# Optimization experiments

Hardware: AMD Instinct MI355X
Metric: run time of the kernel (lower is better)

The kernel has to match this reference:

```python
import jax, jax.numpy as jnp
import numpy as np
import math

B, T, D, H, L = 8, 1024, 128, 8, 2
DH = D // H            # head dim = 16
F = 2 * D              # ffn hidden = 256 (FFN_EXPANSION=2)
SCALE = math.sqrt(DH)  # sqrt of Q last dim per head


def layernorm(x, g, b):
    m = jnp.mean(x, axis=-1, keepdims=True)
    v = jnp.var(x, axis=-1, keepdims=True)
    return (x - m) * jax.lax.rsqrt(v + 1e-5) * g + b


def setup_inputs() -> dict:
    key = jax.random.key(0)
    ks = jax.random.split(key, 16)
    s = 1.0 / math.sqrt(D)
    r = lambda i, shp: jax.random.normal(ks[i], shp, dtype=jnp.float32) * s
    return {
        "x": jax.random.normal(ks[0], (B, T, D), dtype=jnp.float32),
        "y": jax.random.normal(ks[1], (B, T, D), dtype=jnp.float32),
        # shared qkv projections (no bias), per layer
        "Wq": r(2, (L, D, D)), "Wk": r(3, (L, D, D)), "Wv": r(4, (L, D, D)),
        "Wox": r(5, (L, D, D)), "box": jnp.zeros((L, D), jnp.float32),
        "Woy": r(6, (L, D, D)), "boy": jnp.zeros((L, D), jnp.float32),
        "ln1x_g": jnp.ones((L, D), jnp.float32), "ln1x_b": jnp.zeros((L, D), jnp.float32),
        "ln1y_g": jnp.ones((L, D), jnp.float32), "ln1y_b": jnp.zeros((L, D), jnp.float32),
        "ln2x_g": jnp.ones((L, D), jnp.float32), "ln2x_b": jnp.zeros((L, D), jnp.float32),
        "ln2y_g": jnp.ones((L, D), jnp.float32), "ln2y_b": jnp.zeros((L, D), jnp.float32),
        "fx_w1": r(7, (L, D, F)), "fx_b1": jnp.zeros((L, F), jnp.float32),
        "fx_w2": r(8, (L, F, D)), "fx_b2": jnp.zeros((L, D), jnp.float32),
        "fy_w1": r(9, (L, D, F)), "fy_b1": jnp.zeros((L, F), jnp.float32),
        "fy_w2": r(10, (L, F, D)), "fy_b2": jnp.zeros((L, D), jnp.float32),
    }


def _heads(t):
    # (B,T,D) -> (B,T,H,DH)
    return t.reshape(B, T, H, DH)


def _block(x, y, Wq, Wk, Wv, Wox, box, Woy, boy,
           ln1x_g, ln1x_b, ln1y_g, ln1y_b, ln2x_g, ln2x_b, ln2y_g, ln2y_b,
           fx_w1, fx_b1, fx_w2, fx_b2, fy_w1, fy_b1, fy_w2, fy_b2):
    xn = layernorm(x, ln1x_g, ln1x_b)
    yn = layernorm(y, ln1y_g, ln1y_b)
    # x-branch: Q from y, K/V from x ; y-branch: Q from x, K/V from y
    qx = _heads(yn @ Wq); kx = _heads(xn @ Wk); vx = _heads(xn @ Wv)
    qy = _heads(xn @ Wq); ky = _heads(yn @ Wk); vy = _heads(yn @ Wv)
    ax = jnp.einsum('bthd,bshd->bhts', qx, kx)  # (B,H,T,T)
    ay = jnp.einsum('bthd,bshd->bhts', qy, ky)
    # cat over heads + reshape(B,2,H,T,T) + mean(dim=1) == per-head average
    w = jax.nn.softmax((ax + ay) * (0.5 / SCALE), axis=-1)
    o1 = jnp.einsum('bhts,bshd->bthd', w, vx).reshape(B, T, D) @ Wox + box
    o2 = jnp.einsum('bhts,bshd->bthd', w, vy).reshape(B, T, D) @ Woy + boy
    x = x + o1
    y = y + o2
    xn2 = layernorm(x, ln2x_g, ln2x_b)
    yn2 = layernorm(y, ln2y_g, ln2y_b)
    x = x + jax.nn.gelu(xn2 @ fx_w1 + fx_b1, approximate=False) @ fx_w2 + fx_b2
    y = y + jax.nn.gelu(yn2 @ fy_w1 + fy_b1, approximate=False) @ fy_w2 + fy_b2
    return x, y


def reference(x, y, Wq, Wk, Wv, Wox, box, Woy, boy,
              ln1x_g, ln1x_b, ln1y_g, ln1y_b, ln2x_g, ln2x_b, ln2y_g, ln2y_b,
              fx_w1, fx_b1, fx_w2, fx_b2, fy_w1, fy_b1, fy_w2, fy_b2):
    for i in range(L):
        x, y = _block(x, y, Wq[i], Wk[i], Wv[i], Wox[i], box[i], Woy[i], boy[i],
                      ln1x_g[i], ln1x_b[i], ln1y_g[i], ln1y_b[i],
                      ln2x_g[i], ln2x_b[i], ln2y_g[i], ln2y_b[i],
                      fx_w1[i], fx_b1[i], fx_w2[i], fx_b2[i],
                      fy_w1[i], fy_b1[i], fy_w2[i], fy_b2[i])
    return (x, y)
```

## Files before the change

kernel.cpp:

```cpp
#include <hip/hip_runtime.h>
#include <cstddef>

#define BB   8
#define TT   1024
#define DDIM 128
#define HH   8
#define DHH  16
#define FF   256
#define BT   (BB * TT)

typedef unsigned short u16;
typedef __attribute__((ext_vector_type(8))) short short8;
typedef __attribute__((ext_vector_type(4))) float f32x4;

__device__ __forceinline__ u16 bf(float x) {
  unsigned u = __builtin_bit_cast(unsigned, x);
  u += 0x7fffu + ((u >> 16) & 1u);
  return (u16)(u >> 16);
}
__device__ __forceinline__ u16 bft(float x) {
  return (u16)(__builtin_bit_cast(unsigned, x) >> 16);
}
__device__ __forceinline__ float gelu_f(float x) {
  const float t = x * (0.79788456f + 0.03567740814f * x * x);
  return x / (1.0f + __expf(-2.0f * t));
}

struct PrepP { const float* W; u16* Wt; int K; int N; };
struct PrepArgs { PrepP p[18]; };

__global__ __launch_bounds__(256) void prep_k(PrepArgs a) {
  const PrepP pp = a.p[blockIdx.z];
  const int n0 = blockIdx.x * 64, k0 = blockIdx.y * 64;
  if (n0 >= pp.N || k0 >= pp.K) return;
  __shared__ float tile[64][65];
  const int tid = threadIdx.x;
  #pragma unroll
  for (int t = tid; t < 1024; t += 256) {
    const int kk = t >> 4, nn4 = (t & 15) << 2;
    float4 v = *(const float4*)(pp.W + (size_t)(k0 + kk) * pp.N + n0 + nn4);
    tile[nn4 + 0][kk] = v.x; tile[nn4 + 1][kk] = v.y;
    tile[nn4 + 2][kk] = v.z; tile[nn4 + 3][kk] = v.w;
  }
  __syncthreads();
  #pragma unroll
  for (int t = tid; t < 1024; t += 256) {
    const int nn = t >> 4, kk4 = (t & 15) << 2;
    ushort4 o;
    o.x = bf(tile[nn][kk4 + 0]); o.y = bf(tile[nn][kk4 + 1]);
    o.z = bf(tile[nn][kk4 + 2]); o.w = bf(tile[nn][kk4 + 3]);
    *(ushort4*)(pp.Wt + (size_t)(n0 + nn) * pp.K + k0 + kk4) = o;
  }
}

__global__ __launch_bounds__(256) void ln0_k(const float* __restrict__ X,
                                             const float* __restrict__ Y,
                                             const float* __restrict__ gx,
                                             const float* __restrict__ bx,
                                             const float* __restrict__ gy,
                                             const float* __restrict__ by,
                                             u16* __restrict__ ox,
                                             u16* __restrict__ oy) {
  const int which = blockIdx.y;
  const float* in = which ? Y : X;
  const float* g  = which ? gy : gx;
  const float* b  = which ? by : bx;
  u16* out        = which ? oy : ox;
  const int row  = blockIdx.x * 4 + (threadIdx.x >> 6);
  const int lane = threadIdx.x & 63;

  float2 v = *(const float2*)(in + (size_t)row * DDIM + lane * 2);
  float s  = v.x + v.y;
  float sq = v.x * v.x + v.y * v.y;
  #pragma unroll
  for (int off = 32; off >= 1; off >>= 1) {
    s  += __shfl_xor(s, off);
    sq += __shfl_xor(sq, off);
  }
  const float mean = s * (1.0f / DDIM);
  const float var  = sq * (1.0f / DDIM) - mean * mean;
  const float r    = rsqrtf(var + 1e-5f);
  float2 gg = *(const float2*)(g + lane * 2);
  float2 bb = *(const float2*)(b + lane * 2);
  ushort2 o;
  o.x = bf((v.x - mean) * r * gg.x + bb.x);
  o.y = bf((v.y - mean) * r * gg.y + bb.y);
  *(ushort2*)(out + (size_t)row * DDIM + lane * 2) = o;
}

struct GemmP { const u16* A; const u16* Wt; const float* bias; const float* res;
               float* outF; u16* outB; const float* g; const float* b; u16* outT; };
struct GemmArgs { GemmP p[6]; int ln; };

__global__ __launch_bounds__(256) void gemmf_k(GemmArgs a) {
  const GemmP pp = a.p[blockIdx.z];
  const int m0 = blockIdx.y * 32;
  __shared__ __align__(16) u16 As[32][136];
  __shared__ __align__(16) u16 Bs[128][136];
  __shared__ float2 stats[32][2];
  const int tid  = threadIdx.x;
  const int w    = tid >> 6;
  const int lane = tid & 63;
  const int l15  = lane & 15;
  const int quad = lane >> 4;
  const int wr = w & 1, wc = w >> 1;

  f32x4 acc[4];
  #pragma unroll
  for (int j = 0; j < 4; ++j) acc[j] = {0.f, 0.f, 0.f, 0.f};

  #pragma unroll
  for (int t = tid; t < 512; t += 256) {
    const int r = t >> 4, g8 = (t & 15) << 3;
    *(short8*)&As[r][g8] = *(const short8*)(pp.A + (size_t)(m0 + r) * 128 + g8);
  }
  #pragma unroll
  for (int t = tid; t < 2048; t += 256) {
    const int r = t >> 4, g8 = (t & 15) << 3;
    *(short8*)&Bs[r][g8] = *(const short8*)(pp.Wt + (size_t)r * 128 + g8);
  }
  __syncthreads();
  #pragma unroll
  for (int ks = 0; ks < 4; ++ks) {
    const short8 ar = *(const short8*)&As[wr * 16 + l15][ks * 32 + quad * 8];
    #pragma unroll
    for (int j = 0; j < 4; ++j) {
      const short8 br = *(const short8*)&Bs[wc * 64 + j * 16 + l15][ks * 32 + quad * 8];
      acc[j] = __builtin_amdgcn_mfma_f32_16x16x32_bf16(ar, br, acc[j], 0, 0, 0);
    }
  }

  if (pp.outT) {
    const int m_base = m0 + wr * 16 + quad * 4;
    const int bb_ = m_base >> 10, s = m_base & 1023;
    #pragma unroll
    for (int j = 0; j < 4; ++j) {
      const int n = wc * 64 + j * 16 + l15;
      const int h = n >> 4, c = n & 15;
      ushort4 o;
      o.x = bf(acc[j][0]); o.y = bf(acc[j][1]);
      o.z = bf(acc[j][2]); o.w = bf(acc[j][3]);
      *(ushort4*)(pp.outT + (((size_t)(bb_ * 8 + h) * 16 + c) << 10) + s) = o;
    }
    return;
  }

  #pragma unroll
  for (int j = 0; j < 4; ++j) {
    const int n = wc * 64 + j * 16 + l15;
    const float bias_v = pp.bias ? pp.bias[n] : 0.f;
    #pragma unroll
    for (int reg = 0; reg < 4; ++reg) {
      const int m = m0 + wr * 16 + quad * 4 + reg;
      float v = acc[j][reg] + bias_v;
      if (pp.res) v += pp.res[(size_t)m * 128 + n];
      acc[j][reg] = v;
      if (pp.outF) pp.outF[(size_t)m * 128 + n] = v;
    }
  }

  if (!a.ln) {
    if (pp.outB) {
      #pragma unroll
      for (int j = 0; j < 4; ++j) {
        const int n = wc * 64 + j * 16 + l15;
        #pragma unroll
        for (int reg = 0; reg < 4; ++reg) {
          const int m = m0 + wr * 16 + quad * 4 + reg;
          pp.outB[(size_t)m * 128 + n] = bf(acc[j][reg]);
        }
      }
    }
    return;
  }

  #pragma unroll
  for (int reg = 0; reg < 4; ++reg) {
    float s = 0.f, q = 0.f;
    #pragma unroll
    for (int j = 0; j < 4; ++j) { const float v = acc[j][reg]; s += v; q += v * v; }
    #pragma unroll
    for (int off = 8; off >= 1; off >>= 1) {
      s += __shfl_xor(s, off, 16);
      q += __shfl_xor(q, off, 16);
    }
    if (l15 == 0) stats[wr * 16 + quad * 4 + reg][wc] = make_float2(s, q);
  }
  __syncthreads();
  #pragma unroll
  for (int reg = 0; reg < 4; ++reg) {
    const int mloc = wr * 16 + quad * 4 + reg;
    const float2 s0 = stats[mloc][0], s1 = stats[mloc][1];
    const float mean = (s0.x + s1.x) * (1.0f / 128.f);
    const float var  = (s0.y + s1.y) * (1.0f / 128.f) - mean * mean;
    const float r    = rsqrtf(var + 1e-5f);
    #pragma unroll
    for (int j = 0; j < 4; ++j) {
      const int n = wc * 64 + j * 16 + l15;
      pp.outB[(size_t)(m0 + mloc) * 128 + n] =
          bf((acc[j][reg] - mean) * r * pp.g[n] + pp.b[n]);
    }
  }
}

struct FfnP { const u16* A; const u16* W1t; const float* b1;
              const u16* W2t; const float* b2; const float* res;
              float* outF; u16* outB; const float* g; const float* b; };
struct FfnArgs { FfnP p[2]; int ln; };

__global__ __launch_bounds__(256) void ffn_k(FfnArgs a) {
  const FfnP pp = a.p[blockIdx.y];
  const int m0 = blockIdx.x * 32;
  __shared__ __align__(16) u16 As[32][136];
  __shared__ __align__(16) u16 Bs[128][136];
  __shared__ __align__(16) u16 Hs[32][264];
  __shared__ float2 stats[32][2];
  const int tid  = threadIdx.x;
  const int w    = tid >> 6;
  const int lane = tid & 63;
  const int l15  = lane & 15;
  const int quad = lane >> 4;
  const int wr = w & 1, wc = w >> 1;

  #pragma unroll
  for (int t = tid; t < 512; t += 256) {
    const int r = t >> 4, g8 = (t & 15) << 3;
    *(short8*)&As[r][g8] = *(const short8*)(pp.A + (size_t)(m0 + r) * 128 + g8);
  }

  for (int nh = 0; nh < 2; ++nh) {
    #pragma unroll
    for (int t = tid; t < 2048; t += 256) {
      const int r = t >> 4, g8 = (t & 15) << 3;
      *(short8*)&Bs[r][g8] = *(const short8*)(pp.W1t + (size_t)(nh * 128 + r) * 128 + g8);
    }
    __syncthreads();
    f32x4 acc[4];
    #pragma unroll
    for (int j = 0; j < 4; ++j) acc[j] = {0.f, 0.f, 0.f, 0.f};
    #pragma unroll
    for (int ks = 0; ks < 4; ++ks) {
      const short8 ar = *(const short8*)&As[wr * 16 + l15][ks * 32 + quad * 8];
      #pragma unroll
      for (int j = 0; j < 4; ++j) {
        const short8 br = *(const short8*)&Bs[wc * 64 + j * 16 + l15][ks * 32 + quad * 8];
        acc[j] = __builtin_amdgcn_mfma_f32_16x16x32_bf16(ar, br, acc[j], 0, 0, 0);
      }
    }
    #pragma unroll
    for (int j = 0; j < 4; ++j) {
      const int n = wc * 64 + j * 16 + l15;
      const float bias_v = pp.b1[nh * 128 + n];
      #pragma unroll
      for (int reg = 0; reg < 4; ++reg) {
        const int mloc = wr * 16 + quad * 4 + reg;
        Hs[mloc][nh * 128 + n] = bf(gelu_f(acc[j][reg] + bias_v));
      }
    }
    __syncthreads();
  }

  f32x4 acc2[4];
  #pragma unroll
  for (int j = 0; j < 4; ++j) acc2[j] = {0.f, 0.f, 0.f, 0.f};
  for (int kh = 0; kh < 2; ++kh) {
    #pragma unroll
    for (int t = tid; t < 2048; t += 256) {
      const int r = t >> 4, g8 = (t & 15) << 3;
      *(short8*)&Bs[r][g8] = *(const short8*)(pp.W2t + (size_t)r * 256 + kh * 128 + g8);
    }
    __syncthreads();
    #pragma unroll
    for (int ks = 0; ks < 4; ++ks) {
      const short8 ar = *(const short8*)&Hs[wr * 16 + l15][kh * 128 + ks * 32 + quad * 8];
      #pragma unroll
      for (int j = 0; j < 4; ++j) {
        const short8 br = *(const short8*)&Bs[wc * 64 + j * 16 + l15][ks * 32 + quad * 8];
        acc2[j] = __builtin_amdgcn_mfma_f32_16x16x32_bf16(ar, br, acc2[j], 0, 0, 0);
      }
    }
    __syncthreads();
  }

  #pragma unroll
  for (int j = 0; j < 4; ++j) {
    const int n = wc * 64 + j * 16 + l15;
    const float bias_v = pp.b2[n];
    #pragma unroll
    for (int reg = 0; reg < 4; ++reg) {
      const int m = m0 + wr * 16 + quad * 4 + reg;
      float v = acc2[j][reg] + bias_v + pp.res[(size_t)m * 128 + n];
      acc2[j][reg] = v;
      pp.outF[(size_t)m * 128 + n] = v;
    }
  }
  if (!a.ln) return;
  #pragma unroll
  for (int reg = 0; reg < 4; ++reg) {
    float s = 0.f, q = 0.f;
    #pragma unroll
    for (int j = 0; j < 4; ++j) { const float v = acc2[j][reg]; s += v; q += v * v; }
    #pragma unroll
    for (int off = 8; off >= 1; off >>= 1) {
      s += __shfl_xor(s, off, 16);
      q += __shfl_xor(q, off, 16);
    }
    if (l15 == 0) stats[wr * 16 + quad * 4 + reg][wc] = make_float2(s, q);
  }
  __syncthreads();
  #pragma unroll
  for (int reg = 0; reg < 4; ++reg) {
    const int mloc = wr * 16 + quad * 4 + reg;
    const float2 s0 = stats[mloc][0], s1 = stats[mloc][1];
    const float mean = (s0.x + s1.x) * (1.0f / 128.f);
    const float var  = (s0.y + s1.y) * (1.0f / 128.f) - mean * mean;
    const float r    = rsqrtf(var + 1e-5f);
    #pragma unroll
    for (int j = 0; j < 4; ++j) {
      const int n = wc * 64 + j * 16 + l15;
      pp.outB[(size_t)(m0 + mloc) * 128 + n] =
          bf((acc2[j][reg] - mean) * r * pp.g[n] + pp.b[n]);
    }
  }
}

__global__ __launch_bounds__(256) void attn_k(const u16* __restrict__ qx,
                                              const u16* __restrict__ kx,
                                              const u16* __restrict__ qy,
                                              const u16* __restrict__ ky,
                                              const u16* __restrict__ vtx,
                                              const u16* __restrict__ vty,
                                              u16* __restrict__ o1,
                                              u16* __restrict__ o2) {
  const int t0 = blockIdx.x * 64;
  const int bh = blockIdx.y;
  const int b = bh >> 3, h = bh & 7;
  const size_t base = (size_t)b * TT * DDIM + h * DHH;

  __shared__ __align__(16) u16 Ks[2][64][40];
  __shared__ __align__(16) u16 Vt[2][32][72];
  __shared__ __align__(16) u16 Ps[64][72];

  const int tid  = threadIdx.x;
  const int w    = tid >> 6;
  const int lane = tid & 63;
  const int l15  = lane & 15;
  const int quad = lane >> 4;

  const u16* qp = (quad < 2) ? qx : qy;
  const int dq = (quad & 1) * 8;
  const short8 qa = *(const short8*)(qp + base + (size_t)(t0 + w * 16 + l15) * DDIM + dq);

  f32x4 Of0 = {0.f, 0.f, 0.f, 0.f};
  f32x4 Of1 = {0.f, 0.f, 0.f, 0.f};
  float l_i = 0.f;

  const int ks_s = tid >> 2, ks_c = tid & 3;
  const u16* ks_p = (ks_c < 2) ? kx : ky;
  const int ks_d8 = (ks_c & 1) * 8;
  const int ks_col = (ks_c < 2 ? 0 : 16) + ks_d8;

  const int vs_c = tid >> 3;
  const int vs_s8 = (tid & 7) * 8;
  const u16* vs_row = (vs_c < 16) ? (vtx + (((size_t)bh * 16 + vs_c) << 10))
                                  : (vty + (((size_t)bh * 16 + (vs_c - 16)) << 10));

  #define STAGE(kt, buf)                                                          \
    do {                                                                          \
      const int s0_ = (kt) * 64;                                                  \
      *(short8*)&Ks[buf][ks_s][ks_col] =                                          \
          *(const short8*)(ks_p + base + (size_t)(s0_ + ks_s) * DDIM + ks_d8);    \
      *(short8*)&Vt[buf][vs_c][vs_s8] = *(const short8*)(vs_row + s0_ + vs_s8);   \
    } while (0)

  STAGE(0, 0);

  for (int kt = 0; kt < TT / 64; ++kt) {
    const int buf = kt & 1;
    __syncthreads();
    if (kt + 1 < TT / 64) STAGE(kt + 1, buf ^ 1);

    f32x4 Sf[4];
    #pragma unroll
    for (int t = 0; t < 4; ++t) {
      short8 kb = *(const short8*)&Ks[buf][t * 16 + l15][quad * 8];
      f32x4 z = {0.f, 0.f, 0.f, 0.f};
      Sf[t] = __builtin_amdgcn_mfma_f32_16x16x32_bf16(kb, qa, z, 0, 0, 0);
    }

    #pragma unroll
    for (int t = 0; t < 4; ++t) {
      const float p0 = exp2f(Sf[t][0] * 0.18033688011112042f);
      const float p1 = exp2f(Sf[t][1] * 0.18033688011112042f);
      const float p2 = exp2f(Sf[t][2] * 0.18033688011112042f);
      const float p3 = exp2f(Sf[t][3] * 0.18033688011112042f);
      l_i += p0 + p1 + p2 + p3;
      ushort4 pk;
      pk.x = bft(p0); pk.y = bft(p1); pk.z = bft(p2); pk.w = bft(p3);
      *(ushort4*)&Ps[w * 16 + l15][t * 16 + quad * 4] = pk;
    }

    #pragma unroll
    for (int sh = 0; sh < 2; ++sh) {
      short8 pa  = *(const short8*)&Ps[w * 16 + l15][sh * 32 + quad * 8];
      short8 vb0 = *(const short8*)&Vt[buf][l15][sh * 32 + quad * 8];
      short8 vb1 = *(const short8*)&Vt[buf][16 + l15][sh * 32 + quad * 8];
      Of0 = __builtin_amdgcn_mfma_f32_16x16x32_bf16(pa, vb0, Of0, 0, 0, 0);
      Of1 = __builtin_amdgcn_mfma_f32_16x16x32_bf16(pa, vb1, Of1, 0, 0, 0);
    }
  }
  #undef STAGE

  l_i += __shfl_xor(l_i, 16);
  l_i += __shfl_xor(l_i, 32);
  #pragma unroll
  for (int reg = 0; reg < 4; ++reg) {
    const float lq = __shfl(l_i, quad * 4 + reg, 16);
    const float inv = 1.0f / lq;
    const size_t r = base + (size_t)(t0 + w * 16 + quad * 4 + reg) * DDIM + l15;
    o1[r] = bf(Of0[reg] * inv);
    o2[r] = bf(Of1[reg] * inv);
  }
}

extern "C" void kernel_launch(void* const* d_in, const int* in_sizes, int n_in,
                              void* d_out, int out_size, void* d_ws, size_t ws_size,
                              hipStream_t stream) {
  const float* x_in  = (const float*)d_in[0];
  const float* y_in  = (const float*)d_in[1];
  const float* Wq    = (const float*)d_in[2];
  const float* Wk    = (const float*)d_in[3];
  const float* Wv    = (const float*)d_in[4];
  const float* Wox   = (const float*)d_in[5];
  const float* box   = (const float*)d_in[6];
  const float* Woy   = (const float*)d_in[7];
  const float* boy   = (const float*)d_in[8];
  const float* ln1xg = (const float*)d_in[9];
  const float* ln1xb = (const float*)d_in[10];
  const float* ln1yg = (const float*)d_in[11];
  const float* ln1yb = (const float*)d_in[12];
  const float* ln2xg = (const float*)d_in[13];
  const float* ln2xb = (const float*)d_in[14];
  const float* ln2yg = (const float*)d_in[15];
  const float* ln2yb = (const float*)d_in[16];
  const float* fxw1  = (const float*)d_in[17];
  const float* fxb1  = (const float*)d_in[18];
  const float* fxw2  = (const float*)d_in[19];
  const float* fxb2  = (const float*)d_in[20];
  const float* fyw1  = (const float*)d_in[21];
  const float* fyb1  = (const float*)d_in[22];
  const float* fyw2  = (const float*)d_in[23];
  const float* fyb2  = (const float*)d_in[24];

  const size_t S = (size_t)BT * DDIM;
  float* X = (float*)d_out;
  float* Y = X + S;

  char* wsb = (char*)d_ws;
  auto carve = [&](size_t bytes) { char* p = wsb; wsb += (bytes + 255) & ~(size_t)255; return p; };
  u16* xn  = (u16*)carve(S * 2);
  u16* yn  = (u16*)carve(S * 2);
  u16* qx  = (u16*)carve(S * 2);
  u16* kx  = (u16*)carve(S * 2);
  u16* qy  = (u16*)carve(S * 2);
  u16* ky  = (u16*)carve(S * 2);
  u16* vxT = (u16*)carve(S * 2);
  u16* vyT = (u16*)carve(S * 2);
  u16* ob1 = (u16*)carve(S * 2);
  u16* ob2 = (u16*)carve(S * 2);
  u16* WqT[2], *WkT[2], *WvT[2], *WoxT[2], *WoyT[2];
  u16* f1xT[2], *f1yT[2], *f2xT[2], *f2yT[2];
  for (int l = 0; l < 2; ++l) {
    WqT[l]  = (u16*)carve(16384 * 2);
    WkT[l]  = (u16*)carve(16384 * 2);
    WvT[l]  = (u16*)carve(16384 * 2);
    WoxT[l] = (u16*)carve(16384 * 2);
    WoyT[l] = (u16*)carve(16384 * 2);
    f1xT[l] = (u16*)carve(32768 * 2);
    f1yT[l] = (u16*)carve(32768 * 2);
    f2xT[l] = (u16*)carve(32768 * 2);
    f2yT[l] = (u16*)carve(32768 * 2);
  }

  {
    PrepArgs a;
    int idx = 0;
    for (int l = 0; l < 2; ++l) {
      a.p[idx++] = {Wq  + (size_t)l * 16384, WqT[l],  128, 128};
      a.p[idx++] = {Wk  + (size_t)l * 16384, WkT[l],  128, 128};
      a.p[idx++] = {Wv  + (size_t)l * 16384, WvT[l],  128, 128};
      a.p[idx++] = {Wox + (size_t)l * 16384, WoxT[l], 128, 128};
      a.p[idx++] = {Woy + (size_t)l * 16384, WoyT[l], 128, 128};
      a.p[idx++] = {fxw1 + (size_t)l * 32768, f1xT[l], 128, 256};
      a.p[idx++] = {fyw1 + (size_t)l * 32768, f1yT[l], 128, 256};
      a.p[idx++] = {fxw2 + (size_t)l * 32768, f2xT[l], 256, 128};
      a.p[idx++] = {fyw2 + (size_t)l * 32768, f2yT[l], 256, 128};
    }
    prep_k<<<dim3(4, 4, 18), 256, 0, stream>>>(a);
  }

  ln0_k<<<dim3(BT / 4, 2), 256, 0, stream>>>(x_in, y_in, ln1xg, ln1xb, ln1yg, ln1yb, xn, yn);

  for (int l = 0; l < 2; ++l) {
    const size_t bo  = (size_t)l * DDIM;
    const size_t fbo = (size_t)l * FF;

    {
      GemmArgs a = {}; a.ln = 0;
      a.p[0] = {yn, WqT[l], nullptr, nullptr, nullptr, qx, nullptr, nullptr, nullptr};
      a.p[1] = {xn, WkT[l], nullptr, nullptr, nullptr, kx, nullptr, nullptr, nullptr};
      a.p[2] = {xn, WvT[l], nullptr, nullptr, nullptr, nullptr, nullptr, nullptr, vxT};
      a.p[3] = {xn, WqT[l], nullptr, nullptr, nullptr, qy, nullptr, nullptr, nullptr};
      a.p[4] = {yn, WkT[l], nullptr, nullptr, nullptr, ky, nullptr, nullptr, nullptr};
      a.p[5] = {yn, WvT[l], nullptr, nullptr, nullptr, nullptr, nullptr, nullptr, vyT};
      gemmf_k<<<dim3(1, BT / 32, 6), 256, 0, stream>>>(a);
    }
    attn_k<<<dim3(TT / 64, BB * HH), 256, 0, stream>>>(qx, kx, qy, ky, vxT, vyT, ob1, ob2);
    {
      const float* resx = (l == 0) ? x_in : X;
      const float* resy = (l == 0) ? y_in : Y;
      GemmArgs a = {}; a.ln = 1;
      a.p[0] = {ob1, WoxT[l], box + bo, resx, X, xn, ln2xg + bo, ln2xb + bo, nullptr};
      a.p[1] = {ob2, WoyT[l], boy + bo, resy, Y, yn, ln2yg + bo, ln2yb + bo, nullptr};
      gemmf_k<<<dim3(1, BT / 32, 2), 256, 0, stream>>>(a);
    }
    {
      FfnArgs a = {}; a.ln = (l == 0) ? 1 : 0;
      if (l == 0) {
        a.p[0] = {xn, f1xT[l], fxb1 + fbo, f2xT[l], fxb2 + bo, X, X, xn,
                  ln1xg + DDIM, ln1xb + DDIM};
        a.p[1] = {yn, f1yT[l], fyb1 + fbo, f2yT[l], fyb2 + bo, Y, Y, yn,
                  ln1yg + DDIM, ln1yb + DDIM};
      } else {
        a.p[0] = {xn, f1xT[l], fxb1 + fbo, f2xT[l], fxb2 + bo, X, X, nullptr,
                  nullptr, nullptr};
        a.p[1] = {yn, f1yT[l], fyb1 + fbo, f2yT[l], fyb2 + bo, Y, Y, nullptr,
                  nullptr, nullptr};
      }
      ffn_k<<<dim3(BT / 32, 2), 256, 0, stream>>>(a);
    }
  }
}
```

Baseline: 251.5 us.

## Fuse output projection with LayerNorm and FFN, merge weight prep with initial LayerNorm

The Wo projection, residual add and second LayerNorm are folded into the FFN kernel. The normalized activations stay in shared memory as the FFN input and the post-attention residual stays in registers, so the intermediate X/Y fp32 and xn/yn bf16 round trips through global memory and one launch per layer go away. Weight transpose/convert and the first LayerNorm are merged into a single setup launch. The fused kernel does more serial work per block and holds more live registers, which may lower occupancy.

```diff
diff --git a/kernel.cpp b/kernel.cpp
--- a/kernel.cpp
+++ b/kernel.cpp
@@ -26,78 +26,80 @@
   return x / (1.0f + __expf(-2.0f * t));
 }
 
-struct PrepP { const float* W; u16* Wt; int K; int N; };
-struct PrepArgs { PrepP p[18]; };
-
-__global__ __launch_bounds__(256) void prep_k(PrepArgs a) {
-  const PrepP pp = a.p[blockIdx.z];
-  const int n0 = blockIdx.x * 64, k0 = blockIdx.y * 64;
-  if (n0 >= pp.N || k0 >= pp.K) return;
+struct PrepP { const float* W; u16* Wt; };
+struct SetupArgs {
+  PrepP prep[18];
+  const float* x_in; const float* y_in;
+  const float* ln1xg; const float* ln1xb; const float* ln1yg; const float* ln1yb;
+  u16* xn; u16* yn;
+};
+
+__global__ __launch_bounds__(256) void setup_k(SetupArgs a) {
   __shared__ float tile[64][65];
+  const int u = blockIdx.x;
   const int tid = threadIdx.x;
-  #pragma unroll
-  for (int t = tid; t < 1024; t += 256) {
-    const int kk = t >> 4, nn4 = (t & 15) << 2;
-    float4 v = *(const float4*)(pp.W + (size_t)(k0 + kk) * pp.N + n0 + nn4);
-    tile[nn4 + 0][kk] = v.x; tile[nn4 + 1][kk] = v.y;
-    tile[nn4 + 2][kk] = v.z; tile[nn4 + 3][kk] = v.w;
-  }
-  __syncthreads();
-  #pragma unroll
-  for (int t = tid; t < 1024; t += 256) {
-    const int nn = t >> 4, kk4 = (t & 15) << 2;
-    ushort4 o;
-    o.x = bf(tile[nn][kk4 + 0]); o.y = bf(tile[nn][kk4 + 1]);
-    o.z = bf(tile[nn][kk4 + 2]); o.w = bf(tile[nn][kk4 + 3]);
-    *(ushort4*)(pp.Wt + (size_t)(n0 + nn) * pp.K + k0 + kk4) = o;
-  }
-}
-
-__global__ __launch_bounds__(256) void ln0_k(const float* __restrict__ X,
-                                             const float* __restrict__ Y,
-                                             const float* __restrict__ gx,
-                                             const float* __restrict__ bx,
-                                             const float* __restrict__ gy,
-                                             const float* __restrict__ by,
-                                             u16* __restrict__ ox,
-                                             u16* __restrict__ oy) {
-  const int which = blockIdx.y;
-  const float* in = which ? Y : X;
-  const float* g  = which ? gy : gx;
-  const float* b  = which ? by : bx;
-  u16* out        = which ? oy : ox;
-  const int row  = blockIdx.x * 4 + (threadIdx.x >> 6);
-  const int lane = threadIdx.x & 63;
-
-  float2 v = *(const float2*)(in + (size_t)row * DDIM + lane * 2);
-  float s  = v.x + v.y;
-  float sq = v.x * v.x + v.y * v.y;
-  #pragma unroll
-  for (int off = 32; off >= 1; off >>= 1) {
-    s  += __shfl_xor(s, off);
-    sq += __shfl_xor(sq, off);
-  }
-  const float mean = s * (1.0f / DDIM);
-  const float var  = sq * (1.0f / DDIM) - mean * mean;
-  const float r    = rsqrtf(var + 1e-5f);
-  float2 gg = *(const float2*)(g + lane * 2);
-  float2 bb = *(const float2*)(b + lane * 2);
-  ushort2 o;
-  o.x = bf((v.x - mean) * r * gg.x + bb.x);
-  o.y = bf((v.y - mean) * r * gg.y + bb.y);
-  *(ushort2*)(out + (size_t)row * DDIM + lane * 2) = o;
-}
-
-struct GemmP { const u16* A; const u16* Wt; const float* bias; const float* res;
-               float* outF; u16* outB; const float* g; const float* b; u16* outT; };
-struct GemmArgs { GemmP p[6]; int ln; };
+  if (u < 104) {
+    int idx, ti, K, N;
+    if (u < 40)      { idx = u >> 2;               ti = u & 3;        K = 128; N = 128; }
+    else if (u < 72) { idx = 10 + ((u - 40) >> 3); ti = (u - 40) & 7; K = 128; N = 256; }
+    else             { idx = 14 + ((u - 72) >> 3); ti = (u - 72) & 7; K = 256; N = 128; }
+    const int n0 = (N == 256) ? (ti & 3) * 64 : (ti & 1) * 64;
+    const int k0 = (N == 256) ? (ti >> 2) * 64 : (ti >> 1) * 64;
+    const PrepP pp = a.prep[idx];
+    #pragma unroll
+    for (int t = tid; t < 1024; t += 256) {
+      const int kk = t >> 4, nn4 = (t & 15) << 2;
+      float4 v = *(const float4*)(pp.W + (size_t)(k0 + kk) * N + n0 + nn4);
+      tile[nn4 + 0][kk] = v.x; tile[nn4 + 1][kk] = v.y;
+      tile[nn4 + 2][kk] = v.z; tile[nn4 + 3][kk] = v.w;
+    }
+    __syncthreads();
+    #pragma unroll
+    for (int t = tid; t < 1024; t += 256) {
+      const int nn = t >> 4, kk4 = (t & 15) << 2;
+      ushort4 o;
+      o.x = bf(tile[nn][kk4 + 0]); o.y = bf(tile[nn][kk4 + 1]);
+      o.z = bf(tile[nn][kk4 + 2]); o.w = bf(tile[nn][kk4 + 3]);
+      *(ushort4*)(pp.Wt + (size_t)(n0 + nn) * K + k0 + kk4) = o;
+    }
+  } else {
+    const int v_ = u - 104;
+    const int which = v_ & 1;
+    const int row   = (v_ >> 1) * 4 + (tid >> 6);
+    const int lane  = tid & 63;
+    const float* in = which ? a.y_in : a.x_in;
+    const float* g  = which ? a.ln1yg : a.ln1xg;
+    const float* b  = which ? a.ln1yb : a.ln1xb;
+    u16* out        = which ? a.yn : a.xn;
+
+    float2 v = *(const float2*)(in + (size_t)row * DDIM + lane * 2);
+    float s  = v.x + v.y;
+    float sq = v.x * v.x + v.y * v.y;
+    #pragma unroll
+    for (int off = 32; off >= 1; off >>= 1) {
+      s  += __shfl_xor(s, off);
+      sq += __shfl_xor(sq, off);
+    }
+    const float mean = s * (1.0f / DDIM);
+    const float var  = sq * (1.0f / DDIM) - mean * mean;
+    const float r    = rsqrtf(var + 1e-5f);
+    float2 gg = *(const float2*)(g + lane * 2);
+    float2 bb = *(const float2*)(b + lane * 2);
+    ushort2 o;
+    o.x = bf((v.x - mean) * r * gg.x + bb.x);
+    o.y = bf((v.y - mean) * r * gg.y + bb.y);
+    *(ushort2*)(out + (size_t)row * DDIM + lane * 2) = o;
+  }
+}
+
+struct GemmP { const u16* A; const u16* Wt; u16* outB; u16* outT; };
+struct GemmArgs { GemmP p[6]; };
 
 __global__ __launch_bounds__(256) void gemmf_k(GemmArgs a) {
   const GemmP pp = a.p[blockIdx.z];
   const int m0 = blockIdx.y * 32;
   __shared__ __align__(16) u16 As[32][136];
   __shared__ __align__(16) u16 Bs[128][136];
-  __shared__ float2 stats[32][2];
   const int tid  = threadIdx.x;
   const int w    = tid >> 6;
   const int lane = tid & 63;
@@ -148,68 +150,23 @@
   #pragma unroll
   for (int j = 0; j < 4; ++j) {
     const int n = wc * 64 + j * 16 + l15;
-    const float bias_v = pp.bias ? pp.bias[n] : 0.f;
     #pragma unroll
     for (int reg = 0; reg < 4; ++reg) {
       const int m = m0 + wr * 16 + quad * 4 + reg;
-      float v = acc[j][reg] + bias_v;
-      if (pp.res) v += pp.res[(size_t)m * 128 + n];
-      acc[j][reg] = v;
-      if (pp.outF) pp.outF[(size_t)m * 128 + n] = v;
-    }
-  }
-
-  if (!a.ln) {
-    if (pp.outB) {
-      #pragma unroll
-      for (int j = 0; j < 4; ++j) {
-        const int n = wc * 64 + j * 16 + l15;
-        #pragma unroll
-        for (int reg = 0; reg < 4; ++reg) {
-          const int m = m0 + wr * 16 + quad * 4 + reg;
-          pp.outB[(size_t)m * 128 + n] = bf(acc[j][reg]);
-        }
-      }
-    }
-    return;
-  }
-
-  #pragma unroll
-  for (int reg = 0; reg < 4; ++reg) {
-    float s = 0.f, q = 0.f;
-    #pragma unroll
-    for (int j = 0; j < 4; ++j) { const float v = acc[j][reg]; s += v; q += v * v; }
-    #pragma unroll
-    for (int off = 8; off >= 1; off >>= 1) {
-      s += __shfl_xor(s, off, 16);
-      q += __shfl_xor(q, off, 16);
-    }
-    if (l15 == 0) stats[wr * 16 + quad * 4 + reg][wc] = make_float2(s, q);
-  }
-  __syncthreads();
-  #pragma unroll
-  for (int reg = 0; reg < 4; ++reg) {
-    const int mloc = wr * 16 + quad * 4 + reg;
-    const float2 s0 = stats[mloc][0], s1 = stats[mloc][1];
-    const float mean = (s0.x + s1.x) * (1.0f / 128.f);
-    const float var  = (s0.y + s1.y) * (1.0f / 128.f) - mean * mean;
-    const float r    = rsqrtf(var + 1e-5f);
-    #pragma unroll
-    for (int j = 0; j < 4; ++j) {
-      const int n = wc * 64 + j * 16 + l15;
-      pp.outB[(size_t)(m0 + mloc) * 128 + n] =
-          bf((acc[j][reg] - mean) * r * pp.g[n] + pp.b[n]);
-    }
-  }
-}
-
-struct FfnP { const u16* A; const u16* W1t; const float* b1;
-              const u16* W2t; const float* b2; const float* res;
-              float* outF; u16* outB; const float* g; const float* b; };
-struct FfnArgs { FfnP p[2]; int ln; };
-
-__global__ __launch_bounds__(256) void ffn_k(FfnArgs a) {
-  const FfnP pp = a.p[blockIdx.y];
+      pp.outB[(size_t)m * 128 + n] = bf(acc[j][reg]);
+    }
+  }
+}
+
+struct WofnP { const u16* A; const u16* WoT; const float* bo; const float* res;
+               const float* g2; const float* b2l;
+               const u16* W1t; const float* b1;
+               const u16* W2t; const float* b2;
+               float* outF; u16* outB; const float* gn; const float* bn; };
+struct WofnArgs { WofnP p[2]; int ln; };
+
+__global__ __launch_bounds__(256) void wofn_k(WofnArgs a) {
+  const WofnP pp = a.p[blockIdx.y];
   const int m0 = blockIdx.x * 32;
   __shared__ __align__(16) u16 As[32][136];
   __shared__ __align__(16) u16 Bs[128][136];
@@ -227,6 +184,64 @@
     const int r = t >> 4, g8 = (t & 15) << 3;
     *(short8*)&As[r][g8] = *(const short8*)(pp.A + (size_t)(m0 + r) * 128 + g8);
   }
+  #pragma unroll
+  for (int t = tid; t < 2048; t += 256) {
+    const int r = t >> 4, g8 = (t & 15) << 3;
+    *(short8*)&Bs[r][g8] = *(const short8*)(pp.WoT + (size_t)r * 128 + g8);
+  }
+  __syncthreads();
+  f32x4 acc[4];
+  #pragma unroll
+  for (int j = 0; j < 4; ++j) acc[j] = {0.f, 0.f, 0.f, 0.f};
+  #pragma unroll
+  for (int ks = 0; ks < 4; ++ks) {
+    const short8 ar = *(const short8*)&As[wr * 16 + l15][ks * 32 + quad * 8];
+    #pragma unroll
+    for (int j = 0; j < 4; ++j) {
+      const short8 br = *(const short8*)&Bs[wc * 64 + j * 16 + l15][ks * 32 + quad * 8];
+      acc[j] = __builtin_amdgcn_mfma_f32_16x16x32_bf16(ar, br, acc[j], 0, 0, 0);
+    }
+  }
+
+  float xv[4][4];
+  #pragma unroll
+  for (int j = 0; j < 4; ++j) {
+    const int n = wc * 64 + j * 16 + l15;
+    const float bias_v = pp.bo[n];
+    #pragma unroll
+    for (int reg = 0; reg < 4; ++reg) {
+      const int m = m0 + wr * 16 + quad * 4 + reg;
+      xv[j][reg] = acc[j][reg] + bias_v + pp.res[(size_t)m * 128 + n];
+    }
+  }
+
+  #pragma unroll
+  for (int reg = 0; reg < 4; ++reg) {
+    float s = 0.f, q = 0.f;
+    #pragma unroll
+    for (int j = 0; j < 4; ++j) { const float v = xv[j][reg]; s += v; q += v * v; }
+    #pragma unroll
+    for (int off = 8; off >= 1; off >>= 1) {
+      s += __shfl_xor(s, off, 16);
+      q += __shfl_xor(q, off, 16);
+    }
+    if (l15 == 0) stats[wr * 16 + quad * 4 + reg][wc] = make_float2(s, q);
+  }
+  __syncthreads();
+  #pragma unroll
+  for (int reg = 0; reg < 4; ++reg) {
+    const int mloc = wr * 16 + quad * 4 + reg;
+    const float2 s0 = stats[mloc][0], s1 = stats[mloc][1];
+    const float mean = (s0.x + s1.x) * (1.0f / 128.f);
+    const float var  = (s0.y + s1.y) * (1.0f / 128.f) - mean * mean;
+    const float r    = rsqrtf(var + 1e-5f);
+    #pragma unroll
+    for (int j = 0; j < 4; ++j) {
+      const int n = wc * 64 + j * 16 + l15;
+      As[mloc][n] = bf((xv[j][reg] - mean) * r * pp.g2[n] + pp.b2l[n]);
+    }
+  }
+  __syncthreads();
 
   for (int nh = 0; nh < 2; ++nh) {
     #pragma unroll
@@ -235,16 +250,16 @@
       *(short8*)&Bs[r][g8] = *(const short8*)(pp.W1t + (size_t)(nh * 128 + r) * 128 + g8);
     }
     __syncthreads();
-    f32x4 acc[4];
-    #pragma unroll
-    for (int j = 0; j < 4; ++j) acc[j] = {0.f, 0.f, 0.f, 0.f};
+    f32x4 a1[4];
+    #pragma unroll
+    for (int j = 0; j < 4; ++j) a1[j] = {0.f, 0.f, 0.f, 0.f};
     #pragma unroll
     for (int ks = 0; ks < 4; ++ks) {
       const short8 ar = *(const short8*)&As[wr * 16 + l15][ks * 32 + quad * 8];
       #pragma unroll
       for (int j = 0; j < 4; ++j) {
         const short8 br = *(const short8*)&Bs[wc * 64 + j * 16 + l15][ks * 32 + quad * 8];
-        acc[j] = __builtin_amdgcn_mfma_f32_16x16x32_bf16(ar, br, acc[j], 0, 0, 0);
+        a1[j] = __builtin_amdgcn_mfma_f32_16x16x32_bf16(ar, br, a1[j], 0, 0, 0);
       }
     }
     #pragma unroll
@@ -254,15 +269,15 @@
       #pragma unroll
       for (int reg = 0; reg < 4; ++reg) {
         const int mloc = wr * 16 + quad * 4 + reg;
-        Hs[mloc][nh * 128 + n] = bf(gelu_f(acc[j][reg] + bias_v));
+        Hs[mloc][nh * 128 + n] = bf(gelu_f(a1[j][reg] + bias_v));
       }
     }
     __syncthreads();
   }
 
-  f32x4 acc2[4];
-  #pragma unroll
-  for (int j = 0; j < 4; ++j) acc2[j] = {0.f, 0.f, 0.f, 0.f};
+  f32x4 a2[4];
+  #pragma unroll
+  for (int j = 0; j < 4; ++j) a2[j] = {0.f, 0.f, 0.f, 0.f};
   for (int kh = 0; kh < 2; ++kh) {
     #pragma unroll
     for (int t = tid; t < 2048; t += 256) {
@@ -276,7 +291,7 @@
       #pragma unroll
       for (int j = 0; j < 4; ++j) {
         const short8 br = *(const short8*)&Bs[wc * 64 + j * 16 + l15][ks * 32 + quad * 8];
-        acc2[j] = __builtin_amdgcn_mfma_f32_16x16x32_bf16(ar, br, acc2[j], 0, 0, 0);
+        a2[j] = __builtin_amdgcn_mfma_f32_16x16x32_bf16(ar, br, a2[j], 0, 0, 0);
       }
     }
     __syncthreads();
@@ -289,8 +304,8 @@
     #pragma unroll
     for (int reg = 0; reg < 4; ++reg) {
       const int m = m0 + wr * 16 + quad * 4 + reg;
-      float v = acc2[j][reg] + bias_v + pp.res[(size_t)m * 128 + n];
-      acc2[j][reg] = v;
+      const float v = a2[j][reg] + bias_v + xv[j][reg];
+      xv[j][reg] = v;
       pp.outF[(size_t)m * 128 + n] = v;
     }
   }
@@ -299,7 +314,7 @@
   for (int reg = 0; reg < 4; ++reg) {
     float s = 0.f, q = 0.f;
     #pragma unroll
-    for (int j = 0; j < 4; ++j) { const float v = acc2[j][reg]; s += v; q += v * v; }
+    for (int j = 0; j < 4; ++j) { const float v = xv[j][reg]; s += v; q += v * v; }
     #pragma unroll
     for (int off = 8; off >= 1; off >>= 1) {
       s += __shfl_xor(s, off, 16);
@@ -319,7 +334,7 @@
     for (int j = 0; j < 4; ++j) {
       const int n = wc * 64 + j * 16 + l15;
       pp.outB[(size_t)(m0 + mloc) * 128 + n] =
-          bf((acc2[j][reg] - mean) * r * pp.g[n] + pp.b[n]);
+          bf((xv[j][reg] - mean) * r * pp.gn[n] + pp.bn[n]);
     }
   }
 }
@@ -483,61 +498,57 @@
   }
 
   {
-    PrepArgs a;
-    int idx = 0;
+    SetupArgs a;
+    int pi = 0;
     for (int l = 0; l < 2; ++l) {
-      a.p[idx++] = {Wq  + (size_t)l * 16384, WqT[l],  128, 128};
-      a.p[idx++] = {Wk  + (size_t)l * 16384, WkT[l],  128, 128};
-      a.p[idx++] = {Wv  + (size_t)l * 16384, WvT[l],  128, 128};
-      a.p[idx++] = {Wox + (size_t)l * 16384, WoxT[l], 128, 128};
-      a.p[idx++] = {Woy + (size_t)l * 16384, WoyT[l], 128, 128};
-      a.p[idx++] = {fxw1 + (size_t)l * 32768, f1xT[l], 128, 256};
-      a.p[idx++] = {fyw1 + (size_t)l * 32768, f1yT[l], 128, 256};
-      a.p[idx++] = {fxw2 + (size_t)l * 32768, f2xT[l], 256, 128};
-      a.p[idx++] = {fyw2 + (size_t)l * 32768, f2yT[l], 256, 128};
-    }
-    prep_k<<<dim3(4, 4, 18), 256, 0, stream>>>(a);
-  }
-
-  ln0_k<<<dim3(BT / 4, 2), 256, 0, stream>>>(x_in, y_in, ln1xg, ln1xb, ln1yg, ln1yb, xn, yn);
+      a.prep[pi++] = {Wq  + (size_t)l * 16384, WqT[l]};
+      a.prep[pi++] = {Wk  + (size_t)l * 16384, WkT[l]};
+      a.prep[pi++] = {Wv  + (size_t)l * 16384, WvT[l]};
+      a.prep[pi++] = {Wox + (size_t)l * 16384, WoxT[l]};
+      a.prep[pi++] = {Woy + (size_t)l * 16384, WoyT[l]};
+    }
+    for (int l = 0; l < 2; ++l) {
+      a.prep[pi++] = {fxw1 + (size_t)l * 32768, f1xT[l]};
+      a.prep[pi++] = {fyw1 + (size_t)l * 32768, f1yT[l]};
+    }
+    for (int l = 0; l < 2; ++l) {
+      a.prep[pi++] = {fxw2 + (size_t)l * 32768, f2xT[l]};
+      a.prep[pi++] = {fyw2 + (size_t)l * 32768, f2yT[l]};
+    }
+    a.x_in = x_in; a.y_in = y_in;
+    a.ln1xg = ln1xg; a.ln1xb = ln1xb; a.ln1yg = ln1yg; a.ln1yb = ln1yb;
+    a.xn = xn; a.yn = yn;
+    setup_k<<<dim3(104 + 4096), 256, 0, stream>>>(a);
+  }
 
   for (int l = 0; l < 2; ++l) {
     const size_t bo  = (size_t)l * DDIM;
     const size_t fbo = (size_t)l * FF;
 
     {
-      GemmArgs a = {}; a.ln = 0;
-      a.p[0] = {yn, WqT[l], nullptr, nullptr, nullptr, qx, nullptr, nullptr, nullptr};
-      a.p[1] = {xn, WkT[l], nullptr, nullptr, nullptr, kx, nullptr, nullptr, nullptr};
-      a.p[2] = {xn, WvT[l], nullptr, nullptr, nullptr, nullptr, nullptr, nullptr, vxT};
-      a.p[3] = {xn, WqT[l], nullptr, nullptr, nullptr, qy, nullptr, nullptr, nullptr};
-      a.p[4] = {yn, WkT[l], nullptr, nullptr, nullptr, ky, nullptr, nullptr, nullptr};
-      a.p[5] = {yn, WvT[l], nullptr, nullptr, nullptr, nullptr, nullptr, nullptr, vyT};
+      GemmArgs a = {};
+      a.p[0] = {yn, WqT[l], qx, nullptr};
+      a.p[1] = {xn, WkT[l], kx, nullptr};
+      a.p[2] = {xn, WvT[l], nullptr, vxT};
+      a.p[3] = {xn, WqT[l], qy, nullptr};
+      a.p[4] = {yn, WkT[l], ky, nullptr};
+      a.p[5] = {yn, WvT[l], nullptr, vyT};
       gemmf_k<<<dim3(1, BT / 32, 6), 256, 0, stream>>>(a);
     }
     attn_k<<<dim3(TT / 64, BB * HH), 256, 0, stream>>>(qx, kx, qy, ky, vxT, vyT, ob1, ob2);
     {
       const float* resx = (l == 0) ? x_in : X;
       const float* resy = (l == 0) ? y_in : Y;
-      GemmArgs a = {}; a.ln = 1;
-      a.p[0] = {ob1, WoxT[l], box + bo, resx, X, xn, ln2xg + bo, ln2xb + bo, nullptr};
-      a.p[1] = {ob2, WoyT[l], boy + bo, resy, Y, yn, ln2yg + bo, ln2yb + bo, nullptr};
-      gemmf_k<<<dim3(1, BT / 32, 2), 256, 0, stream>>>(a);
-    }
-    {
-      FfnArgs a = {}; a.ln = (l == 0) ? 1 : 0;
-      if (l == 0) {
-        a.p[0] = {xn, f1xT[l], fxb1 + fbo, f2xT[l], fxb2 + bo, X, X, xn,
-                  ln1xg + DDIM, ln1xb + DDIM};
-        a.p[1] = {yn, f1yT[l], fyb1 + fbo, f2yT[l], fyb2 + bo, Y, Y, yn,
-                  ln1yg + DDIM, ln1yb + DDIM};
-      } else {
-        a.p[0] = {xn, f1xT[l], fxb1 + fbo, f2xT[l], fxb2 + bo, X, X, nullptr,
-                  nullptr, nullptr};
-        a.p[1] = {yn, f1yT[l], fyb1 + fbo, f2yT[l], fyb2 + bo, Y, Y, nullptr,
-                  nullptr, nullptr};
-      }
-      ffn_k<<<dim3(BT / 32, 2), 256, 0, stream>>>(a);
-    }
-  }
-}
+      WofnArgs a = {}; a.ln = (l == 0) ? 1 : 0;
+      a.p[0] = {ob1, WoxT[l], box + bo, resx, ln2xg + bo, ln2xb + bo,
+                f1xT[l], fxb1 + fbo, f2xT[l], fxb2 + bo,
+                X, (l == 0) ? xn : nullptr,
+                (l == 0) ? ln1xg + DDIM : nullptr, (l == 0) ? ln1xb + DDIM : nullptr};
+      a.p[1] = {ob2, WoyT[l], boy + bo, resy, ln2yg + bo, ln2yb + bo,
+                f1yT[l], fyb1 + fbo, f2yT[l], fyb2 + bo,
+                Y, (l == 0) ? yn : nullptr,
+                (l == 0) ? ln1yg + DDIM : nullptr, (l == 0) ? ln1yb + DDIM : nullptr};
+      wofn_k<<<dim3(BT / 32, 2), 256, 0, stream>>>(a);
+    }
+  }
+}
```

New measurement: 226.4 us. -10.0%, faster.
